# Performance work log

Hardware: AMD Instinct MI355X
Metric: run time of the kernel (lower is better)

## Reference

```python
import jax, jax.numpy as jnp
import numpy as np

B = 32      # graphs per batch
N_NODES = 1024  # nodes per graph
K = 16      # top-k edges per node


def setup_inputs() -> dict:
    key = jax.random.key(0)
    k1, k2 = jax.random.split(key)
    x = jax.random.normal(k1, (B * N_NODES, 128), dtype=jnp.float32) * 0.1
    W = jax.random.normal(k2, (128, 64), dtype=jnp.float32) * (1.0 / np.sqrt(128))
    b = jnp.zeros((64,), dtype=jnp.float32)
    temperature = jnp.asarray(4.0, dtype=jnp.float32)
    return {"x": x, "W": W, "b": b, "temperature": temperature}


def reference(x, W, b, temperature):
    # Encoder: linear node embedding. out: [B*n, C]
    out = x @ W + b
    C = out.shape[-1]
    # Per-graph features, detached as in the original (graph_x = out[...].detach())
    h = jax.lax.stop_gradient(out).reshape(B, N_NODES, C)
    # Pairwise squared euclidean distances per graph: d[b,i,j] = ||h_i - h_j||^2
    sq = jnp.sum(h * h, axis=-1)  # [B, n]
    d_e = sq[:, :, None] + sq[:, None, :] - 2.0 * jnp.einsum('bic,bjc->bij', h, h)
    logits = jnp.exp(-temperature * d_e)  # [B, n, n]
    # Gumbel-noised top-k edge sampling
    z = jax.random.gumbel(jax.random.key(1), logits.shape, logits.dtype)
    _, edges_hat = jax.lax.top_k(logits + z, K)  # [B, n, K] int32
    # Build global edge index with cumulative per-graph node offsets
    offsets = (jnp.arange(B, dtype=jnp.int32) * N_NODES)[:, None, None]  # [B,1,1]
    rows = jnp.broadcast_to(jnp.arange(N_NODES, dtype=jnp.int32)[None, :, None] + offsets,
                            (B, N_NODES, K))
    cols = edges_hat.astype(jnp.int32) + offsets
    edges_idx = jnp.stack((rows.reshape(-1), cols.reshape(-1)))  # [2, B*n*K]
    return out, edges_idx
```

## Files before the change

### kernel.cpp

```cpp
#include <hip/hip_runtime.h>
#include <math.h>

#define OUT_ELEMS 2097152
#define EDGE_ELEMS 524288

__device__ __forceinline__ unsigned int rotl32(unsigned int x, int r){
  return (x << r) | (x >> (32 - r));
}

__device__ __forceinline__ unsigned int tf_bits_part(unsigned int e){
  unsigned int x0 = 0u, x1 = e;
  const unsigned int ks1 = 1u;
  const unsigned int ks2 = 0x1BD11BDBu;
  x1 += ks1;
#define TFR(r) { x0 += x1; x1 = rotl32(x1, r); x1 ^= x0; }
  TFR(13) TFR(15) TFR(26) TFR(6)
  x0 += ks1; x1 += ks2 + 1u;
  TFR(17) TFR(29) TFR(16) TFR(24)
  x0 += ks2; x1 += 0u + 2u;
  TFR(13) TFR(15) TFR(26) TFR(6)
  x0 += 0u;  x1 += ks1 + 3u;
  TFR(17) TFR(29) TFR(16) TFR(24)
  x0 += ks1; x1 += ks2 + 4u;
  TFR(13) TFR(15) TFR(26) TFR(6)
  x0 += ks2; x1 += 0u + 5u;
#undef TFR
  return x0 ^ x1;
}

__device__ __forceinline__ double rcp64(double x){
  double r;
  asm("v_rcp_f64 %0, %1" : "=v"(r) : "v"(x));
  double e = fma(-x, r, 1.0); r = fma(r, e, r);
  e = fma(-x, r, 1.0); r = fma(r, e, r);
  return r;
}

__device__ __forceinline__ double fast_exp(double x){
  double fn = __builtin_rint(x * 1.4426950408889634);
  int n = (int)fn;
  double r = fma(fn, -0.6931471803691238, x);
  r = fma(fn, -1.9082149292705877e-10, r);
  double p = 2.7557319223985893e-06;
  p = fma(r, p, 2.4801587301587302e-05);
  p = fma(r, p, 1.9841269841269841e-04);
  p = fma(r, p, 1.3888888888888889e-03);
  p = fma(r, p, 8.3333333333333333e-03);
  p = fma(r, p, 4.1666666666666664e-02);
  p = fma(r, p, 1.6666666666666666e-01);
  p = fma(r, p, 0.5);
  p = fma(r, p, 1.0);
  p = fma(r, p, 1.0);
  double scale = __longlong_as_double(((long long)(n + 1023)) << 52);
  return p * scale;
}

__device__ __forceinline__ double fast_log(double x){
  long long bx = __double_as_longlong(x);
  long long e = (bx >> 52) - 1023;
  double m = __longlong_as_double((bx & 0xFFFFFFFFFFFFFll) |
                                  0x3FF0000000000000ll);
  int big = m > 1.4142135623730951;
  m = big ? 0.5 * m : m;
  e += big;
  double s = (m - 1.0) * rcp64(m + 1.0);
  double s2 = s * s;
  double p = fma(s2, 2.0/11.0, 2.0/9.0);
  p = fma(s2, p, 2.0/7.0);
  p = fma(s2, p, 2.0/5.0);
  p = fma(s2, p, 2.0/3.0);
  double lm = fma(s * s2, p, 2.0 * s);
  return fma((double)e, 0.6931471805599453, lm);
}

__device__ __forceinline__ unsigned long long score_cand(
    const float* __restrict__ og, const double* __restrict__ hrow,
    unsigned int jc, unsigned int base, double Td, bool act){
  const float4* cp4 = (const float4*)(og + ((size_t)jc << 6));
  double acc = 0.0;
  #pragma unroll 4
  for (int ch = 0; ch < 16; ++ch){
    float4 cf = cp4[ch];
    double d0 = hrow[(ch << 2) + 0] - (double)cf.x;
    double d1 = hrow[(ch << 2) + 1] - (double)cf.y;
    double d2 = hrow[(ch << 2) + 2] - (double)cf.z;
    double d3 = hrow[(ch << 2) + 3] - (double)cf.w;
    acc = fma(d0, d0, acc);
    acc = fma(d1, d1, acc);
    acc = fma(d2, d2, acc);
    acc = fma(d3, d3, acc);
  }
  if (!act) return 0ull;
  double sgm = fast_exp(-Td * acc);
  unsigned int bits = tf_bits_part(base | jc);
  float f = __uint_as_float(0x3f800000u | (bits >> 9)) - 1.0f;
  double u = (f > 0.0f) ? (double)f : 1.1754943508222875e-38;
  double w = -fast_log(u);
  double z = -fast_log(w);
  double sc = sgm + z;
  unsigned long long kb = (unsigned long long)__double_as_longlong(sc);
  kb ^= (unsigned long long)(((long long)kb) >> 63) | 0x8000000000000000ull;
  return (kb & ~1023ull) | (unsigned long long)(1023u - jc);
}

__device__ __forceinline__ unsigned long long bitonic64_desc(
    unsigned long long key, int lane){
  #pragma unroll
  for (int k = 2; k <= 64; k <<= 1){
    #pragma unroll
    for (int j = k >> 1; j; j >>= 1){
      unsigned long long o = __shfl_xor(key, j, 64);
      bool keep_hi = ((lane & k) == 0) == ((lane & j) == 0);
      key = (keep_hi == (o > key)) ? o : key;
    }
  }
  return key;
}

__device__ __forceinline__ unsigned int bitonic32_desc(
    unsigned int key, int lane){
  #pragma unroll
  for (int k = 2; k <= 64; k <<= 1){
    #pragma unroll
    for (int j = k >> 1; j; j >>= 1){
      unsigned int o = __shfl_xor(key, j, 64);
      bool keep_hi = ((lane & k) == 0) == ((lane & j) == 0);
      key = (keep_hi == (o > key)) ? o : key;
    }
  }
  return key;
}

__global__ __launch_bounds__(256) void encoder_v11(
    const float* __restrict__ x, const float* __restrict__ W,
    const float* __restrict__ b, float* __restrict__ out){
  const int tid = threadIdx.x;
  const int wu  = __builtin_amdgcn_readfirstlane(tid >> 6);
  const int c   = tid & 63;
  const size_t r0 = ((size_t)blockIdx.x << 5) + ((size_t)wu << 3);
  const float* __restrict__ xr = x + (r0 << 7);

  double acc[8];
  const double bc = (double)b[c];
  #pragma unroll
  for (int i = 0; i < 8; ++i) acc[i] = bc;

  #pragma unroll 4
  for (int k = 0; k < 128; ++k){
    const double wk = (double)W[(k << 6) + c];
    #pragma unroll
    for (int i = 0; i < 8; ++i)
      acc[i] = fma((double)xr[((size_t)i << 7) + k], wk, acc[i]);
  }

  #pragma unroll
  for (int i = 0; i < 8; ++i)
    out[((r0 + i) << 6) + c] = (float)acc[i];
}

__global__ __launch_bounds__(256, 8) void edges_v11(
    const float* __restrict__ out32, const float* __restrict__ temp,
    float* __restrict__ rows_out, float* __restrict__ cols_out){
  __shared__ double hid[4][64];
  __shared__ unsigned int cl[4][128];
  const int tid = threadIdx.x, wave = tid >> 6, lane = tid & 63;
  const int gb = blockIdx.x >> 8;
  const int i0 = (blockIdx.x & 255) << 2;
  const int r  = i0 + wave;
  const float* __restrict__ og = out32 + ((size_t)gb << 16);

  hid[wave][lane] = (double)og[((size_t)r << 6) + lane];

  const unsigned int base = ((unsigned int)gb << 20) | ((unsigned int)r << 10);

  unsigned int v[16];
  unsigned int pmax = 0u;
  #pragma unroll
  for (int m = 0; m < 16; ++m){
    const unsigned int j = (unsigned int)(m << 6) + (unsigned int)lane;
    unsigned int bits = tf_bits_part(base | j);
    v[m] = (bits & ~1023u) | (1023u - j);
    pmax = (v[m] > pmax) ? v[m] : pmax;
  }

  unsigned int sorted = bitonic32_desc(pmax, lane);
  unsigned int b16p = __shfl(sorted, 15, 64);

  float u16 = __uint_as_float(0x3f800000u | (b16p >> 9)) - 1.0f;
  float z16 = -__logf(-__logf(u16));
  float uc  = __expf(-__expf(-(z16 - 1.001f)));
  unsigned int cp = ((__float_as_uint(1.0f + uc) & 0x7FFFFFu) << 9) & ~1023u;

  int cnt = 0;
  #pragma unroll
  for (int m = 0; m < 16; ++m) cnt += (v[m] >= cp) ? 1 : 0;
  int s = cnt;
  #pragma unroll
  for (int off = 1; off < 64; off <<= 1){
    int o = __shfl_up(s, off, 64);
    s += (lane >= off) ? o : 0;
  }
  int nc = __shfl(s, 63, 64);
  nc = (nc > 128) ? 128 : nc;
  int slot = s - cnt;
  #pragma unroll
  for (int m = 0; m < 16; ++m){
    if (v[m] >= cp && slot < 128){
      cl[wave][slot] = 1023u - (v[m] & 1023u);
      ++slot;
    }
  }

  const double Td = (double)temp[0];
  const bool act1 = (lane < nc);
  unsigned int jc1 = act1 ? cl[wave][lane] : 0u;
  unsigned long long key = score_cand(og, hid[wave], jc1, base, Td, act1);
  key = bitonic64_desc(key, lane);

  if (nc > 64){
    const int idx2 = 64 + lane;
    const bool act2 = (idx2 < nc);
    unsigned int jc2 = act2 ? cl[wave][idx2] : 0u;
    unsigned long long k2 = score_cand(og, hid[wave], jc2, base, Td, act2);
    k2 = bitonic64_desc(k2, lane);
    unsigned long long kr = __shfl(k2, 63 - lane, 64);
    key = (kr > key) ? kr : key;
    #pragma unroll
    for (int j = 32; j; j >>= 1){
      unsigned long long o = __shfl_xor(key, j, 64);
      bool left = (lane & j) == 0;
      bool take = left ? (o > key) : (o < key);
      key = take ? o : key;
    }
  }

  const int grow = (gb << 10) + r;
  if (lane < 16){
    rows_out[((size_t)grow << 4) + lane] = (float)grow;
    cols_out[((size_t)grow << 4) + lane] =
        (float)((gb << 10) + (1023 - (int)(key & 1023ull)));
  }
}

extern "C" void kernel_launch(void* const* d_in, const int* in_sizes, int n_in,
                              void* d_out, int out_size, void* d_ws, size_t ws_size,
                              hipStream_t stream){
  const float* x = (const float*)d_in[0];
  const float* W = (const float*)d_in[1];
  const float* b = (const float*)d_in[2];
  const float* T = (const float*)d_in[3];
  float* out      = (float*)d_out;
  float* rows_out = out + OUT_ELEMS;
  float* cols_out = rows_out + EDGE_ELEMS;

  encoder_v11<<<1024, 256, 0, stream>>>(x, W, b, out);
  edges_v11<<<8192, 256, 0, stream>>>(out, T, rows_out, cols_out);
}
```

Before: 197.1 us.

## Move Gumbel candidate prefilter into encoder launch to overlap with GEMM

The random-bits candidate prefilter depends only on the PRNG, not on the embeddings, so it now runs inside the encoder kernel. Blocks are interleaved at a ratio of one encoder block to eight candidate blocks, so the ALU-heavy threefry work overlaps the encoder's FP64 GEMM. Candidate lists and counts go to workspace memory as ushort arrays, and the scoring kernel reads them back. This adds global writes and reads of the candidate lists, plus a lower occupancy bound on the fused kernel.

```diff
diff --git a/kernel.cpp b/kernel.cpp
--- a/kernel.cpp
+++ b/kernel.cpp
@@ -3,6 +3,8 @@
 
 #define OUT_ELEMS 2097152
 #define EDGE_ELEMS 524288
+#define NROWS 32768
+#define CAND_STRIDE 128
 
 __device__ __forceinline__ unsigned int rotl32(unsigned int x, int r){
   return (x << r) | (x >> (32 - r));
@@ -131,38 +133,94 @@
   return key;
 }
 
-__global__ __launch_bounds__(256) void encoder_v11(
+__global__ __launch_bounds__(256, 4) void fused_enc_cand_v12(
     const float* __restrict__ x, const float* __restrict__ W,
-    const float* __restrict__ b, float* __restrict__ out){
+    const float* __restrict__ b, float* __restrict__ out,
+    unsigned short* __restrict__ cand, unsigned int* __restrict__ cntg){
+  const unsigned int bid = blockIdx.x;
+  const unsigned int q = bid / 9u;
+  const unsigned int t = bid - q * 9u;
   const int tid = threadIdx.x;
-  const int wu  = __builtin_amdgcn_readfirstlane(tid >> 6);
-  const int c   = tid & 63;
-  const size_t r0 = ((size_t)blockIdx.x << 5) + ((size_t)wu << 3);
-  const float* __restrict__ xr = x + (r0 << 7);
-
-  double acc[8];
-  const double bc = (double)b[c];
-  #pragma unroll
-  for (int i = 0; i < 8; ++i) acc[i] = bc;
-
-  #pragma unroll 4
-  for (int k = 0; k < 128; ++k){
-    const double wk = (double)W[(k << 6) + c];
+  const int lane = tid & 63;
+
+  if (t == 0u){
+    const int wu = __builtin_amdgcn_readfirstlane(tid >> 6);
+    const size_t r0 = ((size_t)q << 5) + ((size_t)wu << 3);
+    const float* __restrict__ xr = x + (r0 << 7);
+
+    double acc[8];
+    const double bc = (double)b[lane];
+    #pragma unroll
+    for (int i = 0; i < 8; ++i) acc[i] = bc;
+
+    #pragma unroll 4
+    for (int k = 0; k < 128; ++k){
+      const double wk = (double)W[(k << 6) + lane];
+      #pragma unroll
+      for (int i = 0; i < 8; ++i)
+        acc[i] = fma((double)xr[((size_t)i << 7) + k], wk, acc[i]);
+    }
+
     #pragma unroll
     for (int i = 0; i < 8; ++i)
-      acc[i] = fma((double)xr[((size_t)i << 7) + k], wk, acc[i]);
-  }
-
-  #pragma unroll
-  for (int i = 0; i < 8; ++i)
-    out[((r0 + i) << 6) + c] = (float)acc[i];
-}
-
-__global__ __launch_bounds__(256, 8) void edges_v11(
+      out[((r0 + i) << 6) + lane] = (float)acc[i];
+  } else {
+    const unsigned int cb = (q << 3) + t - 1u;
+    const int wave = tid >> 6;
+    const int gb = (int)(cb >> 8);
+    const int i0 = (int)(cb & 255u) << 2;
+    const int r  = i0 + wave;
+    const unsigned int base = ((unsigned int)gb << 20) | ((unsigned int)r << 10);
+
+    unsigned int v[16];
+    unsigned int pmax = 0u;
+    #pragma unroll
+    for (int m = 0; m < 16; ++m){
+      const unsigned int j = (unsigned int)(m << 6) + (unsigned int)lane;
+      unsigned int bits = tf_bits_part(base | j);
+      v[m] = (bits & ~1023u) | (1023u - j);
+      pmax = (v[m] > pmax) ? v[m] : pmax;
+    }
+
+    unsigned int sorted = bitonic32_desc(pmax, lane);
+    unsigned int b16p = __shfl(sorted, 15, 64);
+
+    float u16v = __uint_as_float(0x3f800000u | (b16p >> 9)) - 1.0f;
+    float z16 = -__logf(-__logf(u16v));
+    float uc  = __expf(-__expf(-(z16 - 1.001f)));
+    unsigned int cp = ((__float_as_uint(1.0f + uc) & 0x7FFFFFu) << 9) & ~1023u;
+
+    int cnt = 0;
+    #pragma unroll
+    for (int m = 0; m < 16; ++m) cnt += (v[m] >= cp) ? 1 : 0;
+    int s = cnt;
+    #pragma unroll
+    for (int off = 1; off < 64; off <<= 1){
+      int o = __shfl_up(s, off, 64);
+      s += (lane >= off) ? o : 0;
+    }
+    int nc = __shfl(s, 63, 64);
+    nc = (nc > 128) ? 128 : nc;
+    int slot = s - cnt;
+    unsigned short* __restrict__ crow =
+        cand + (size_t)(((unsigned int)gb << 10) + (unsigned int)r) * CAND_STRIDE;
+    #pragma unroll
+    for (int m = 0; m < 16; ++m){
+      if (v[m] >= cp && slot < 128){
+        crow[slot] = (unsigned short)(1023u - (v[m] & 1023u));
+        ++slot;
+      }
+    }
+    if (lane == 0) cntg[((unsigned int)gb << 10) + (unsigned int)r] = (unsigned int)nc;
+  }
+}
+
+__global__ __launch_bounds__(256, 8) void edges_score_v12(
     const float* __restrict__ out32, const float* __restrict__ temp,
+    const unsigned short* __restrict__ cand,
+    const unsigned int* __restrict__ cntg,
     float* __restrict__ rows_out, float* __restrict__ cols_out){
   __shared__ double hid[4][64];
-  __shared__ unsigned int cl[4][128];
   const int tid = threadIdx.x, wave = tid >> 6, lane = tid & 63;
   const int gb = blockIdx.x >> 8;
   const int i0 = (blockIdx.x & 255) << 2;
@@ -172,55 +230,20 @@
   hid[wave][lane] = (double)og[((size_t)r << 6) + lane];
 
   const unsigned int base = ((unsigned int)gb << 20) | ((unsigned int)r << 10);
-
-  unsigned int v[16];
-  unsigned int pmax = 0u;
-  #pragma unroll
-  for (int m = 0; m < 16; ++m){
-    const unsigned int j = (unsigned int)(m << 6) + (unsigned int)lane;
-    unsigned int bits = tf_bits_part(base | j);
-    v[m] = (bits & ~1023u) | (1023u - j);
-    pmax = (v[m] > pmax) ? v[m] : pmax;
-  }
-
-  unsigned int sorted = bitonic32_desc(pmax, lane);
-  unsigned int b16p = __shfl(sorted, 15, 64);
-
-  float u16 = __uint_as_float(0x3f800000u | (b16p >> 9)) - 1.0f;
-  float z16 = -__logf(-__logf(u16));
-  float uc  = __expf(-__expf(-(z16 - 1.001f)));
-  unsigned int cp = ((__float_as_uint(1.0f + uc) & 0x7FFFFFu) << 9) & ~1023u;
-
-  int cnt = 0;
-  #pragma unroll
-  for (int m = 0; m < 16; ++m) cnt += (v[m] >= cp) ? 1 : 0;
-  int s = cnt;
-  #pragma unroll
-  for (int off = 1; off < 64; off <<= 1){
-    int o = __shfl_up(s, off, 64);
-    s += (lane >= off) ? o : 0;
-  }
-  int nc = __shfl(s, 63, 64);
-  nc = (nc > 128) ? 128 : nc;
-  int slot = s - cnt;
-  #pragma unroll
-  for (int m = 0; m < 16; ++m){
-    if (v[m] >= cp && slot < 128){
-      cl[wave][slot] = 1023u - (v[m] & 1023u);
-      ++slot;
-    }
-  }
+  const int grow = (gb << 10) + r;
+  const int nc = (int)cntg[grow];
+  const unsigned short* __restrict__ cl = cand + (size_t)grow * CAND_STRIDE;
 
   const double Td = (double)temp[0];
   const bool act1 = (lane < nc);
-  unsigned int jc1 = act1 ? cl[wave][lane] : 0u;
+  unsigned int jc1 = act1 ? (unsigned int)cl[lane] : 0u;
   unsigned long long key = score_cand(og, hid[wave], jc1, base, Td, act1);
   key = bitonic64_desc(key, lane);
 
   if (nc > 64){
     const int idx2 = 64 + lane;
     const bool act2 = (idx2 < nc);
-    unsigned int jc2 = act2 ? cl[wave][idx2] : 0u;
+    unsigned int jc2 = act2 ? (unsigned int)cl[idx2] : 0u;
     unsigned long long k2 = score_cand(og, hid[wave], jc2, base, Td, act2);
     k2 = bitonic64_desc(k2, lane);
     unsigned long long kr = __shfl(k2, 63 - lane, 64);
@@ -234,7 +257,6 @@
     }
   }
 
-  const int grow = (gb << 10) + r;
   if (lane < 16){
     rows_out[((size_t)grow << 4) + lane] = (float)grow;
     cols_out[((size_t)grow << 4) + lane] =
@@ -253,6 +275,11 @@
   float* rows_out = out + OUT_ELEMS;
   float* cols_out = rows_out + EDGE_ELEMS;
 
-  encoder_v11<<<1024, 256, 0, stream>>>(x, W, b, out);
-  edges_v11<<<8192, 256, 0, stream>>>(out, T, rows_out, cols_out);
-}
+  unsigned short* cand = (unsigned short*)d_ws;
+  unsigned int*   cntg = (unsigned int*)((char*)d_ws +
+                          (size_t)NROWS * CAND_STRIDE * sizeof(unsigned short));
+
+  fused_enc_cand_v12<<<9216, 256, 0, stream>>>(x, W, b, out, cand, cntg);
+  edges_score_v12<<<8192, 256, 0, stream>>>(out, T, cand, cntg,
+                                            rows_out, cols_out);
+}
```

Result: slower. 228.0 us (+15.7%).

## Stage x tile in LDS and pre-convert weights to fp64 for encoder

Applied to the files above, without the earlier changes.

Adds a small kernel that converts W and b to double in workspace, then restructures the encoder so each 512-thread block loads a 64-row x tile into padded shared memory. Each lane owns one row and each wave computes 8 output columns, reading wave-uniform fp64 weights instead of reconverting per element. This targets the strided global x reads and repeated float-to-double conversions in the encoder, at the cost of an extra launch, workspace use and a different store pattern. The edges kernel is only renamed.

```diff
diff --git a/kernel.cpp b/kernel.cpp
--- a/kernel.cpp
+++ b/kernel.cpp
@@ -131,34 +131,62 @@
   return key;
 }
 
-__global__ __launch_bounds__(256) void encoder_v11(
-    const float* __restrict__ x, const float* __restrict__ W,
-    const float* __restrict__ b, float* __restrict__ out){
+__global__ __launch_bounds__(256) void cvt_wb_v15(
+    const float* __restrict__ W, const float* __restrict__ b,
+    double* __restrict__ w64, double* __restrict__ b64){
+  const int i = blockIdx.x * 256 + threadIdx.x;
+  if (i < 8192)      w64[i] = (double)W[i];
+  else if (i < 8256) b64[i - 8192] = (double)b[i - 8192];
+}
+
+__global__ __launch_bounds__(512) void encoder_v15(
+    const float* __restrict__ x, const double* __restrict__ w64,
+    const double* __restrict__ b64, float* __restrict__ out){
+  __shared__ float xs[64 * 129];
   const int tid = threadIdx.x;
-  const int wu  = __builtin_amdgcn_readfirstlane(tid >> 6);
-  const int c   = tid & 63;
-  const size_t r0 = ((size_t)blockIdx.x << 5) + ((size_t)wu << 3);
-  const float* __restrict__ xr = x + (r0 << 7);
+
+  {
+    const float4* xg4 = (const float4*)(x + ((size_t)blockIdx.x << 13));
+    #pragma unroll
+    for (int s = 0; s < 4; ++s){
+      const int idx = tid + (s << 9);
+      float4 v = xg4[idx];
+      const int r = idx >> 5, k4 = (idx & 31) << 2;
+      float* p = &xs[r * 129 + k4];
+      p[0] = v.x; p[1] = v.y; p[2] = v.z; p[3] = v.w;
+    }
+  }
+  __syncthreads();
+
+  const int lane = tid & 63;
+  const int wu = __builtin_amdgcn_readfirstlane(tid >> 6);
+  const int c0 = wu << 3;
+  const size_t row = ((size_t)blockIdx.x << 6) + (size_t)lane;
 
   double acc[8];
-  const double bc = (double)b[c];
-  #pragma unroll
-  for (int i = 0; i < 8; ++i) acc[i] = bc;
-
+  const double* __restrict__ bp = b64 + c0;
+  #pragma unroll
+  for (int j = 0; j < 8; ++j) acc[j] = bp[j];
+
+  const float* __restrict__ xrow = &xs[lane * 129];
   #pragma unroll 4
   for (int k = 0; k < 128; ++k){
-    const double wk = (double)W[(k << 6) + c];
-    #pragma unroll
-    for (int i = 0; i < 8; ++i)
-      acc[i] = fma((double)xr[((size_t)i << 7) + k], wk, acc[i]);
-  }
-
-  #pragma unroll
-  for (int i = 0; i < 8; ++i)
-    out[((r0 + i) << 6) + c] = (float)acc[i];
-}
-
-__global__ __launch_bounds__(256, 8) void edges_v11(
+    const double xk = (double)xrow[k];
+    const double* __restrict__ wp = w64 + (k << 6) + c0;
+    #pragma unroll
+    for (int j = 0; j < 8; ++j)
+      acc[j] = fma(xk, wp[j], acc[j]);
+  }
+
+  float* __restrict__ orow = out + (row << 6) + c0;
+  #pragma unroll
+  for (int j2 = 0; j2 < 4; ++j2){
+    float2 st; st.x = (float)acc[(j2 << 1)]; st.y = (float)acc[(j2 << 1) + 1];
+    *(float2*)&orow[j2 << 1] = st;
+  }
+}
+
+__global__ __launch_bounds__(256, 8) void edges_v15(
     const float* __restrict__ out32, const float* __restrict__ temp,
     float* __restrict__ rows_out, float* __restrict__ cols_out){
   __shared__ double hid[4][64];
@@ -253,6 +281,10 @@
   float* rows_out = out + OUT_ELEMS;
   float* cols_out = rows_out + EDGE_ELEMS;
 
-  encoder_v11<<<1024, 256, 0, stream>>>(x, W, b, out);
-  edges_v11<<<8192, 256, 0, stream>>>(out, T, rows_out, cols_out);
-}
+  double* w64 = (double*)d_ws;
+  double* b64 = w64 + 8192;
+
+  cvt_wb_v15<<<33, 256, 0, stream>>>(W, b, w64, b64);
+  encoder_v15<<<512, 512, 0, stream>>>(x, w64, b64, out);
+  edges_v15<<<8192, 256, 0, stream>>>(out, T, rows_out, cols_out);
+}
```

Result: faster. 189.2 us (-4.0%).
